# Performance work log

Measured on AMD Instinct MI355X. Metric: run time of the kernel, lower is better.

Reference implementation:

```python
import jax, jax.numpy as jnp
import numpy as np

N_NODES = 100000
N_EDGES = 1600000
NFEAT = 64
NCLASS = 64


def setup_inputs() -> dict:
    key = jax.random.key(0)
    k1, k2, k3, k4, k5, k6 = jax.random.split(key, 6)
    x = jax.random.normal(k1, (N_NODES, NFEAT), dtype=jnp.float32)
    adj = jax.random.randint(k2, (2, N_EDGES), 0, N_NODES, dtype=jnp.int64)
    # PyG GraphConv params: lin_rel (with bias), lin_root (no bias)
    s_rel = 1.0 / np.sqrt(NFEAT)
    W_rel = jax.random.uniform(k3, (NCLASS, NFEAT), jnp.float32, -s_rel, s_rel)
    b_rel = jax.random.uniform(k4, (NCLASS,), jnp.float32, -s_rel, s_rel)
    W_root = jax.random.uniform(k5, (NCLASS, NFEAT), jnp.float32, -s_rel, s_rel)
    return {"x": x, "adj": adj, "W_rel": W_rel, "b_rel": b_rel, "W_root": W_root}


def reference(x, adj, W_rel, b_rel, W_root):
    src, dst = adj[0], adj[1]
    # sum-aggregate neighbor features: agg[i] = sum_{(j->i)} x[j]
    agg = jax.ops.segment_sum(x[src], dst, num_segments=N_NODES)  # [N, nfeat]
    # GraphConv: lin_rel(agg) + lin_root(x), then ReLU
    out = agg @ W_rel.T + b_rel + x @ W_root.T  # [N, nclass]
    return jax.nn.relu(out)
```

## Files before the change

kernel.cpp:

```cpp
#include <hip/hip_runtime.h>

#define N_NODES 100000
#define N_EDGES 1600000
#define NFEAT 64
#define NCLASS 64
#define NGROUPS (N_NODES / 16)

#define PARTS 511
#define NPP 196
#define BINB 256
#define EPB (N_EDGES / BINB)
#define BCAP 48
#define TCAP 3712

typedef __attribute__((ext_vector_type(8))) short bf16x8;
typedef __attribute__((ext_vector_type(4))) float f32x4;

__device__ inline unsigned short f2bf(float f) {
    union { float f; unsigned u; } v; v.f = f;
    unsigned u = v.u + 0x7fffu + ((v.u >> 16) & 1u);
    return (unsigned short)(u >> 16);
}
__device__ inline float bf2f(unsigned short s) {
    union { unsigned u; float f; } v; v.u = ((unsigned)s) << 16;
    return v.f;
}

#define X_ITEMS (N_NODES * NFEAT / 4)
#define W_ITEMS (NCLASS * 128)
__global__ void prep_kernel(const float4* __restrict__ x4,
                            ushort4* __restrict__ xb4,
                            const float* __restrict__ W_rel,
                            const float* __restrict__ W_root,
                            unsigned short* __restrict__ Wcat) {
    int i = blockIdx.x * blockDim.x + threadIdx.x;
    int stride = gridDim.x * blockDim.x;
    for (; i < X_ITEMS + W_ITEMS; i += stride) {
        if (i < X_ITEMS) {
            float4 v = x4[i];
            ushort4 o;
            o.x = f2bf(v.x); o.y = f2bf(v.y); o.z = f2bf(v.z); o.w = f2bf(v.w);
            xb4[i] = o;
        } else {
            int j = i - X_ITEMS;
            int c = j >> 7, k = j & 127;
            float v = (k < 64) ? W_rel[c * 64 + k] : W_root[c * 64 + (k - 64)];
            Wcat[j] = f2bf(v);
        }
    }
}

__global__ __launch_bounds__(256) void binfine_kernel(const int* __restrict__ src,
                                                      const int* __restrict__ dst,
                                                      int* __restrict__ counts,
                                                      unsigned* __restrict__ staging) {
    __shared__ int cur[PARTS];
    const int blk = blockIdx.x;
    const int tid = threadIdx.x;
    for (int i = tid; i < PARTS; i += 256) cur[i] = 0;
    __syncthreads();
    const int e0 = blk * EPB;
    for (int r = tid; r < EPB; r += 256) {
        int e = e0 + r;
        unsigned d = (unsigned)dst[e];
        unsigned s = (unsigned)src[e];
        unsigned p = d / (unsigned)NPP;
        unsigned dl = d - p * (unsigned)NPP;
        int pos = atomicAdd(&cur[p], 1);
        if (pos < BCAP)
            staging[((size_t)blk * PARTS + p) * BCAP + pos] = (dl << 17) | s;
    }
    __syncthreads();
    for (int i = tid; i < PARTS; i += 256)
        counts[blk * PARTS + i] = min(cur[i], BCAP);
}

__global__ __launch_bounds__(1024) void aggsort_kernel(
    const unsigned short* __restrict__ x_bf,
    const int* __restrict__ counts,
    const unsigned* __restrict__ staging,
    unsigned short* __restrict__ agg_bf) {
    __shared__ unsigned list[TCAP];
    __shared__ unsigned slot[TCAP];
    __shared__ int segorig[BINB], segscan[BINB], segoff[BINB];
    __shared__ int cnt[NPP], nodeoff[NPP], curn[NPP];
    __shared__ int scan256[256];

    const int p = blockIdx.x;
    const int tid = threadIdx.x;

    if (tid < BINB) {
        int c = counts[tid * PARTS + p];
        segorig[tid] = c;
        segscan[tid] = c;
    }
    __syncthreads();
    for (int off = 1; off < BINB; off <<= 1) {
        int v = 0;
        if (tid < BINB && tid >= off) v = segscan[tid - off];
        __syncthreads();
        if (tid < BINB && tid >= off) segscan[tid] += v;
        __syncthreads();
    }
    if (tid < BINB) segoff[tid] = segscan[tid] - segorig[tid];
    __syncthreads();
    const int total = min(segscan[BINB - 1], TCAP);

    for (int k = tid; k < BINB * BCAP; k += 1024) {
        int seg = k / BCAP;
        int idx = k - seg * BCAP;
        if (idx < segorig[seg]) {
            int dp = segoff[seg] + idx;
            if (dp < TCAP)
                list[dp] = staging[((size_t)seg * PARTS + p) * BCAP + idx];
        }
    }
    for (int i = tid; i < NPP; i += 1024) cnt[i] = 0;
    __syncthreads();
    for (int i = tid; i < total; i += 1024)
        atomicAdd(&cnt[list[i] >> 17], 1);
    __syncthreads();
    if (tid < 256) scan256[tid] = (tid < NPP) ? cnt[tid] : 0;
    __syncthreads();
    for (int off = 1; off < 256; off <<= 1) {
        int v = 0;
        if (tid < 256 && tid >= off) v = scan256[tid - off];
        __syncthreads();
        if (tid < 256 && tid >= off) scan256[tid] += v;
        __syncthreads();
    }
    if (tid < NPP) {
        int st = scan256[tid] - cnt[tid];
        nodeoff[tid] = st;
        curn[tid] = st;
    }
    __syncthreads();
    for (int i = tid; i < total; i += 1024) {
        unsigned v = list[i];
        int r = (int)(v >> 17);
        int pos = atomicAdd(&curn[r], 1);
        slot[pos] = v & 0x1FFFFu;
    }
    __syncthreads();
    const int lane = tid & 63;
    const int w = tid >> 6;
    for (int r = w; r < NPP; r += 16) {
        int node = p * NPP + r;
        if (node >= N_NODES) break;
        int beg = nodeoff[r];
        int end = beg + cnt[r];
        float acc = 0.f;
        int j = beg;
        for (; j + 4 <= end; j += 4) {
            int s0 = (int)slot[j + 0];
            int s1 = (int)slot[j + 1];
            int s2 = (int)slot[j + 2];
            int s3 = (int)slot[j + 3];
            float v0 = bf2f(x_bf[(size_t)s0 * 64 + lane]);
            float v1 = bf2f(x_bf[(size_t)s1 * 64 + lane]);
            float v2 = bf2f(x_bf[(size_t)s2 * 64 + lane]);
            float v3 = bf2f(x_bf[(size_t)s3 * 64 + lane]);
            acc += v0; acc += v1; acc += v2; acc += v3;
        }
        for (; j < end; ++j) acc += bf2f(x_bf[(size_t)slot[j] * 64 + lane]);
        agg_bf[(size_t)node * 64 + lane] = f2bf(acc);
    }
}

__global__ __launch_bounds__(256, 2) void transform_mfma_kernel(
    const unsigned short* __restrict__ agg_bf,
    const unsigned short* __restrict__ x_bf,
    const unsigned short* __restrict__ Wcat,
    const float* __restrict__ b_rel,
    float* __restrict__ out) {
    const int lane = threadIdx.x & 63;
    const int lr = lane & 15;
    const int lh = lane >> 4;

    bf16x8 bfr[4][4];
    #pragma unroll
    for (int cg = 0; cg < 4; ++cg)
        #pragma unroll
        for (int kk = 0; kk < 4; ++kk)
            bfr[cg][kk] = *(const bf16x8*)(Wcat + (cg * 16 + lr) * 128 + kk * 32 + lh * 8);

    float bias[4];
    #pragma unroll
    for (int cg = 0; cg < 4; ++cg) bias[cg] = b_rel[cg * 16 + lr];

    int wid = (blockIdx.x * blockDim.x + threadIdx.x) >> 6;
    int nw  = (gridDim.x * blockDim.x) >> 6;

    for (int g = wid; g < NGROUPS; g += nw) {
        const unsigned short* Aa = agg_bf + (size_t)(g * 16 + lr) * 64;
        const unsigned short* Ax = x_bf   + (size_t)(g * 16 + lr) * 64;
        bf16x8 afr[4];
        #pragma unroll
        for (int kk = 0; kk < 2; ++kk) {
            afr[kk]     = *(const bf16x8*)(Aa + kk * 32 + lh * 8);
            afr[kk + 2] = *(const bf16x8*)(Ax + kk * 32 + lh * 8);
        }
        #pragma unroll
        for (int cg = 0; cg < 4; ++cg) {
            f32x4 acc = {0.f, 0.f, 0.f, 0.f};
            #pragma unroll
            for (int kk = 0; kk < 4; ++kk)
                acc = __builtin_amdgcn_mfma_f32_16x16x32_bf16(afr[kk], bfr[cg][kk], acc, 0, 0, 0);
            #pragma unroll
            for (int r = 0; r < 4; ++r)
                out[(size_t)(g * 16 + lh * 4 + r) * 64 + cg * 16 + lr] =
                    fmaxf(acc[r] + bias[cg], 0.f);
        }
    }
}

__global__ void zero_kernel(float4* __restrict__ p, int n4) {
    int i = blockIdx.x * blockDim.x + threadIdx.x;
    int stride = gridDim.x * blockDim.x;
    for (; i < n4; i += stride) p[i] = make_float4(0.f, 0.f, 0.f, 0.f);
}

__global__ void scatter_kernel(const float4* __restrict__ x4,
                               const int* __restrict__ src,
                               const int* __restrict__ dst,
                               float* __restrict__ agg) {
    int idx = blockIdx.x * blockDim.x + threadIdx.x;
    const int total = N_EDGES * 16;
    int stride = gridDim.x * blockDim.x;
    for (; idx < total; idx += stride) {
        int e = idx >> 4;
        int q = idx & 15;
        int s = src[e];
        int d = dst[e];
        float4 v = x4[s * 16 + q];
        float* base = agg + d * 64 + q * 4;
        unsafeAtomicAdd(base + 0, v.x);
        unsafeAtomicAdd(base + 1, v.y);
        unsafeAtomicAdd(base + 2, v.z);
        unsafeAtomicAdd(base + 3, v.w);
    }
}

__global__ __launch_bounds__(256, 1) void transform3_kernel(
    const float* __restrict__ x,
    const float* __restrict__ W_rel,
    const float* __restrict__ b_rel,
    const float* __restrict__ W_root,
    float* __restrict__ agg_out) {
    const int lane = threadIdx.x & 63;
    float4 wr[16], wo[16];
    const float4* Wr4 = (const float4*)W_rel;
    const float4* Wo4 = (const float4*)W_root;
    #pragma unroll
    for (int i = 0; i < 16; ++i) {
        float4 a = Wr4[lane * 16 + i];
        float4 b = Wo4[lane * 16 + i];
        asm volatile("" : "+v"(a.x), "+v"(a.y), "+v"(a.z), "+v"(a.w));
        asm volatile("" : "+v"(b.x), "+v"(b.y), "+v"(b.z), "+v"(b.w));
        wr[i] = a;
        wo[i] = b;
    }
    const float bias = b_rel[lane];
    int gwave = (blockIdx.x * blockDim.x + threadIdx.x) >> 6;
    int nwaves = (gridDim.x * blockDim.x) >> 6;
    for (int node = gwave; node < N_NODES; node += nwaves) {
        const float4* ar4 = (const float4*)(agg_out + (size_t)node * 64);
        const float4* xr4 = (const float4*)(x + (size_t)node * 64);
        float acc = bias;
        #pragma unroll
        for (int i = 0; i < 16; ++i) {
            float4 a = ar4[i];
            float4 v = xr4[i];
            acc += a.x * wr[i].x + a.y * wr[i].y + a.z * wr[i].z + a.w * wr[i].w;
            acc += v.x * wo[i].x + v.y * wo[i].y + v.z * wo[i].z + v.w * wo[i].w;
        }
        agg_out[(size_t)node * 64 + lane] = fmaxf(acc, 0.f);
    }
}

extern "C" void kernel_launch(void* const* d_in, const int* in_sizes, int n_in,
                              void* d_out, int out_size, void* d_ws, size_t ws_size,
                              hipStream_t stream) {
    const float* x      = (const float*)d_in[0];
    const int*   adj    = (const int*)d_in[1];
    const float* W_rel  = (const float*)d_in[2];
    const float* b_rel  = (const float*)d_in[3];
    const float* W_root = (const float*)d_in[4];
    float*       out    = (float*)d_out;

    const int* src = adj;
    const int* dst = adj + N_EDGES;

    const size_t CNT_INTS = (size_t)BINB * PARTS;
    const size_t row_elems = (size_t)N_NODES * 64;
    const size_t bf_base = ((CNT_INTS * sizeof(int)) + 127) & ~(size_t)127;
    const size_t ws_needed = bf_base +
        (2 * row_elems + (size_t)NCLASS * 128) * sizeof(unsigned short);

    if (ws_size >= ws_needed) {
        int* counts = (int*)d_ws;
        unsigned short* x_bf   = (unsigned short*)((char*)d_ws + bf_base);
        unsigned short* agg_bf = x_bf + row_elems;
        unsigned short* Wcat   = agg_bf + row_elems;
        unsigned* staging = (unsigned*)d_out;

        prep_kernel<<<2048, 256, 0, stream>>>((const float4*)x, (ushort4*)x_bf,
                                              W_rel, W_root, Wcat);
        binfine_kernel<<<BINB, 256, 0, stream>>>(src, dst, counts, staging);
        aggsort_kernel<<<PARTS, 1024, 0, stream>>>(x_bf, counts, staging, agg_bf);
        transform_mfma_kernel<<<1024, 256, 0, stream>>>(agg_bf, x_bf, Wcat, b_rel, out);
    } else {
        zero_kernel<<<2048, 256, 0, stream>>>((float4*)out, (N_NODES * NFEAT) / 4);
        scatter_kernel<<<4096, 256, 0, stream>>>((const float4*)x, src, dst, out);
        transform3_kernel<<<1024, 256, 0, stream>>>(x, W_rel, b_rel, W_root, out);
    }
}
```

Before: 91.51 us.

## Fuse transform GEMM into aggregation kernel and merge prep with binning

Merges the bf16 conversion and edge binning into one launch, and fuses the MFMA transform into the aggregation kernel: the aggregated rows stay in shared memory (aggT) instead of round-tripping through an agg_bf buffer in global memory. Staging is laid out per partition inside the output buffer, so each partition block overwrites only its own staging region when it writes out. The last partition uses a workspace area because its output rows are smaller than its staging block. Partition sizes change to 208 nodes (13 MFMA groups of 16). This removes two launches and one global intermediate, but adds shared-memory pressure in a 1024-thread block and runs MFMA in only 13 waves per block.

```diff
diff --git a/kernel.cpp b/kernel.cpp
--- a/kernel.cpp
+++ b/kernel.cpp
@@ -4,14 +4,17 @@
 #define N_EDGES 1600000
 #define NFEAT 64
 #define NCLASS 64
-#define NGROUPS (N_NODES / 16)
-
-#define PARTS 511
-#define NPP 196
+
+#define PARTS 481
+#define NPP 208
+#define NG 13
 #define BINB 256
 #define EPB (N_EDGES / BINB)
-#define BCAP 48
-#define TCAP 3712
+#define BCAP 49
+#define TCAP 3904
+#define SLOT_INTS (NPP * 64)
+#define SEG_INTS (BINB * BCAP)
+#define ATS 72
 
 typedef __attribute__((ext_vector_type(8))) short bf16x8;
 typedef __attribute__((ext_vector_type(4))) float f32x4;
@@ -28,66 +31,74 @@
 
 #define X_ITEMS (N_NODES * NFEAT / 4)
 #define W_ITEMS (NCLASS * 128)
-__global__ void prep_kernel(const float4* __restrict__ x4,
-                            ushort4* __restrict__ xb4,
-                            const float* __restrict__ W_rel,
-                            const float* __restrict__ W_root,
-                            unsigned short* __restrict__ Wcat) {
-    int i = blockIdx.x * blockDim.x + threadIdx.x;
-    int stride = gridDim.x * blockDim.x;
-    for (; i < X_ITEMS + W_ITEMS; i += stride) {
-        if (i < X_ITEMS) {
-            float4 v = x4[i];
-            ushort4 o;
-            o.x = f2bf(v.x); o.y = f2bf(v.y); o.z = f2bf(v.z); o.w = f2bf(v.w);
-            xb4[i] = o;
-        } else {
-            int j = i - X_ITEMS;
-            int c = j >> 7, k = j & 127;
-            float v = (k < 64) ? W_rel[c * 64 + k] : W_root[c * 64 + (k - 64)];
-            Wcat[j] = f2bf(v);
-        }
-    }
-}
-
-__global__ __launch_bounds__(256) void binfine_kernel(const int* __restrict__ src,
-                                                      const int* __restrict__ dst,
-                                                      int* __restrict__ counts,
-                                                      unsigned* __restrict__ staging) {
+__global__ __launch_bounds__(256) void prepbin_kernel(
+    const float4* __restrict__ x4, ushort4* __restrict__ xb4,
+    const float* __restrict__ W_rel, const float* __restrict__ W_root,
+    unsigned short* __restrict__ Wcat,
+    const int* __restrict__ src, const int* __restrict__ dst,
+    int* __restrict__ counts,
+    unsigned* __restrict__ stg_out,
+    unsigned* __restrict__ stg_ws) {
     __shared__ int cur[PARTS];
-    const int blk = blockIdx.x;
     const int tid = threadIdx.x;
-    for (int i = tid; i < PARTS; i += 256) cur[i] = 0;
-    __syncthreads();
-    const int e0 = blk * EPB;
-    for (int r = tid; r < EPB; r += 256) {
-        int e = e0 + r;
-        unsigned d = (unsigned)dst[e];
-        unsigned s = (unsigned)src[e];
-        unsigned p = d / (unsigned)NPP;
-        unsigned dl = d - p * (unsigned)NPP;
-        int pos = atomicAdd(&cur[p], 1);
-        if (pos < BCAP)
-            staging[((size_t)blk * PARTS + p) * BCAP + pos] = (dl << 17) | s;
-    }
-    __syncthreads();
-    for (int i = tid; i < PARTS; i += 256)
-        counts[blk * PARTS + i] = min(cur[i], BCAP);
-}
-
-__global__ __launch_bounds__(1024) void aggsort_kernel(
+    if (blockIdx.x < BINB) {
+        const int blk = blockIdx.x;
+        for (int i = tid; i < PARTS; i += 256) cur[i] = 0;
+        __syncthreads();
+        const int e0 = blk * EPB;
+        for (int r = tid; r < EPB; r += 256) {
+            int e = e0 + r;
+            unsigned d = (unsigned)dst[e];
+            unsigned s = (unsigned)src[e];
+            unsigned p = d / (unsigned)NPP;
+            unsigned dl = d - p * (unsigned)NPP;
+            int pos = atomicAdd(&cur[p], 1);
+            if (pos < BCAP) {
+                unsigned* bp = (p < PARTS - 1) ? stg_out + (size_t)p * SLOT_INTS
+                                               : stg_ws;
+                bp[blk * BCAP + pos] = (dl << 17) | s;
+            }
+        }
+        __syncthreads();
+        for (int i = tid; i < PARTS; i += 256)
+            counts[blk * PARTS + i] = min(cur[i], BCAP);
+    } else {
+        int i = (blockIdx.x - BINB) * 256 + tid;
+        int stride = (gridDim.x - BINB) * 256;
+        for (; i < X_ITEMS + W_ITEMS; i += stride) {
+            if (i < X_ITEMS) {
+                float4 v = x4[i];
+                ushort4 o;
+                o.x = f2bf(v.x); o.y = f2bf(v.y); o.z = f2bf(v.z); o.w = f2bf(v.w);
+                xb4[i] = o;
+            } else {
+                int j = i - X_ITEMS;
+                int c = j >> 7, k = j & 127;
+                float v = (k < 64) ? W_rel[c * 64 + k] : W_root[c * 64 + (k - 64)];
+                Wcat[j] = f2bf(v);
+            }
+        }
+    }
+}
+
+__global__ __launch_bounds__(1024) void aggsort_fused_kernel(
     const unsigned short* __restrict__ x_bf,
     const int* __restrict__ counts,
-    const unsigned* __restrict__ staging,
-    unsigned short* __restrict__ agg_bf) {
+    const unsigned* __restrict__ stg_out,
+    const unsigned* __restrict__ stg_ws,
+    const unsigned short* __restrict__ Wcat,
+    const float* __restrict__ b_rel,
+    float* __restrict__ out) {
     __shared__ unsigned list[TCAP];
     __shared__ unsigned slot[TCAP];
+    __shared__ __align__(16) unsigned short aggT[NPP * ATS];
     __shared__ int segorig[BINB], segscan[BINB], segoff[BINB];
     __shared__ int cnt[NPP], nodeoff[NPP], curn[NPP];
     __shared__ int scan256[256];
 
     const int p = blockIdx.x;
     const int tid = threadIdx.x;
+    const unsigned* sp = (p < PARTS - 1) ? stg_out + (size_t)p * SLOT_INTS : stg_ws;
 
     if (tid < BINB) {
         int c = counts[tid * PARTS + p];
@@ -111,8 +122,7 @@
         int idx = k - seg * BCAP;
         if (idx < segorig[seg]) {
             int dp = segoff[seg] + idx;
-            if (dp < TCAP)
-                list[dp] = staging[((size_t)seg * PARTS + p) * BCAP + idx];
+            if (dp < TCAP) list[dp] = sp[seg * BCAP + idx];
         }
     }
     for (int i = tid; i < NPP; i += 1024) cnt[i] = 0;
@@ -142,11 +152,10 @@
         slot[pos] = v & 0x1FFFFu;
     }
     __syncthreads();
+
     const int lane = tid & 63;
     const int w = tid >> 6;
     for (int r = w; r < NPP; r += 16) {
-        int node = p * NPP + r;
-        if (node >= N_NODES) break;
         int beg = nodeoff[r];
         int end = beg + cnt[r];
         float acc = 0.f;
@@ -163,53 +172,43 @@
             acc += v0; acc += v1; acc += v2; acc += v3;
         }
         for (; j < end; ++j) acc += bf2f(x_bf[(size_t)slot[j] * 64 + lane]);
-        agg_bf[(size_t)node * 64 + lane] = f2bf(acc);
-    }
-}
-
-__global__ __launch_bounds__(256, 2) void transform_mfma_kernel(
-    const unsigned short* __restrict__ agg_bf,
-    const unsigned short* __restrict__ x_bf,
-    const unsigned short* __restrict__ Wcat,
-    const float* __restrict__ b_rel,
-    float* __restrict__ out) {
-    const int lane = threadIdx.x & 63;
-    const int lr = lane & 15;
-    const int lh = lane >> 4;
-
-    bf16x8 bfr[4][4];
-    #pragma unroll
-    for (int cg = 0; cg < 4; ++cg)
-        #pragma unroll
-        for (int kk = 0; kk < 4; ++kk)
-            bfr[cg][kk] = *(const bf16x8*)(Wcat + (cg * 16 + lr) * 128 + kk * 32 + lh * 8);
-
-    float bias[4];
-    #pragma unroll
-    for (int cg = 0; cg < 4; ++cg) bias[cg] = b_rel[cg * 16 + lr];
-
-    int wid = (blockIdx.x * blockDim.x + threadIdx.x) >> 6;
-    int nw  = (gridDim.x * blockDim.x) >> 6;
-
-    for (int g = wid; g < NGROUPS; g += nw) {
-        const unsigned short* Aa = agg_bf + (size_t)(g * 16 + lr) * 64;
-        const unsigned short* Ax = x_bf   + (size_t)(g * 16 + lr) * 64;
-        bf16x8 afr[4];
-        #pragma unroll
-        for (int kk = 0; kk < 2; ++kk) {
-            afr[kk]     = *(const bf16x8*)(Aa + kk * 32 + lh * 8);
-            afr[kk + 2] = *(const bf16x8*)(Ax + kk * 32 + lh * 8);
-        }
-        #pragma unroll
-        for (int cg = 0; cg < 4; ++cg) {
-            f32x4 acc = {0.f, 0.f, 0.f, 0.f};
+        aggT[r * ATS + lane] = f2bf(acc);
+    }
+    __syncthreads();
+
+    if (w < NG) {
+        const int g = w;
+        const int node0 = p * NPP + g * 16;
+        if (node0 < N_NODES) {
+            const int lr = lane & 15;
+            const int lh = lane >> 4;
+            bf16x8 bfr[4][4];
             #pragma unroll
-            for (int kk = 0; kk < 4; ++kk)
-                acc = __builtin_amdgcn_mfma_f32_16x16x32_bf16(afr[kk], bfr[cg][kk], acc, 0, 0, 0);
+            for (int cg = 0; cg < 4; ++cg)
+                #pragma unroll
+                for (int kk = 0; kk < 4; ++kk)
+                    bfr[cg][kk] = *(const bf16x8*)(Wcat + (cg * 16 + lr) * 128 + kk * 32 + lh * 8);
+            float bias[4];
             #pragma unroll
-            for (int r = 0; r < 4; ++r)
-                out[(size_t)(g * 16 + lh * 4 + r) * 64 + cg * 16 + lr] =
-                    fmaxf(acc[r] + bias[cg], 0.f);
+            for (int cg = 0; cg < 4; ++cg) bias[cg] = b_rel[cg * 16 + lr];
+
+            bf16x8 afr[4];
+            afr[0] = *(const bf16x8*)(aggT + (g * 16 + lr) * ATS + lh * 8);
+            afr[1] = *(const bf16x8*)(aggT + (g * 16 + lr) * ATS + 32 + lh * 8);
+            afr[2] = *(const bf16x8*)(x_bf + (size_t)(node0 + lr) * 64 + lh * 8);
+            afr[3] = *(const bf16x8*)(x_bf + (size_t)(node0 + lr) * 64 + 32 + lh * 8);
+
+            #pragma unroll
+            for (int cg = 0; cg < 4; ++cg) {
+                f32x4 acc = {0.f, 0.f, 0.f, 0.f};
+                #pragma unroll
+                for (int kk = 0; kk < 4; ++kk)
+                    acc = __builtin_amdgcn_mfma_f32_16x16x32_bf16(afr[kk], bfr[cg][kk], acc, 0, 0, 0);
+                #pragma unroll
+                for (int rr = 0; rr < 4; ++rr)
+                    out[(size_t)(node0 + lh * 4 + rr) * 64 + cg * 16 + lr] =
+                        fmaxf(acc[rr] + bias[cg], 0.f);
+            }
         }
     }
 }
@@ -291,24 +290,24 @@
     const int* src = adj;
     const int* dst = adj + N_EDGES;
 
-    const size_t CNT_INTS = (size_t)BINB * PARTS;
+    const size_t n_ints = (size_t)BINB * PARTS + SEG_INTS;
     const size_t row_elems = (size_t)N_NODES * 64;
-    const size_t bf_base = ((CNT_INTS * sizeof(int)) + 127) & ~(size_t)127;
+    const size_t bf_base = ((n_ints * sizeof(int)) + 127) & ~(size_t)127;
     const size_t ws_needed = bf_base +
-        (2 * row_elems + (size_t)NCLASS * 128) * sizeof(unsigned short);
+        (row_elems + (size_t)NCLASS * 128) * sizeof(unsigned short);
 
     if (ws_size >= ws_needed) {
         int* counts = (int*)d_ws;
-        unsigned short* x_bf   = (unsigned short*)((char*)d_ws + bf_base);
-        unsigned short* agg_bf = x_bf + row_elems;
-        unsigned short* Wcat   = agg_bf + row_elems;
-        unsigned* staging = (unsigned*)d_out;
-
-        prep_kernel<<<2048, 256, 0, stream>>>((const float4*)x, (ushort4*)x_bf,
-                                              W_rel, W_root, Wcat);
-        binfine_kernel<<<BINB, 256, 0, stream>>>(src, dst, counts, staging);
-        aggsort_kernel<<<PARTS, 1024, 0, stream>>>(x_bf, counts, staging, agg_bf);
-        transform_mfma_kernel<<<1024, 256, 0, stream>>>(agg_bf, x_bf, Wcat, b_rel, out);
+        unsigned* stg_ws = (unsigned*)d_ws + (size_t)BINB * PARTS;
+        unsigned short* x_bf = (unsigned short*)((char*)d_ws + bf_base);
+        unsigned short* Wcat = x_bf + row_elems;
+        unsigned* stg_out = (unsigned*)d_out;
+
+        prepbin_kernel<<<BINB + 2048, 256, 0, stream>>>(
+            (const float4*)x, (ushort4*)x_bf, W_rel, W_root, Wcat,
+            src, dst, counts, stg_out, stg_ws);
+        aggsort_fused_kernel<<<PARTS, 1024, 0, stream>>>(
+            x_bf, counts, stg_out, stg_ws, Wcat, b_rel, out);
     } else {
         zero_kernel<<<2048, 256, 0, stream>>>((float4*)out, (N_NODES * NFEAT) / 4);
         scatter_kernel<<<4096, 256, 0, stream>>>((const float4*)x, src, dst, out);
```

Measured after the change: 120.6 us. 31.8% more time.
